# Kernel tuning notes

Hardware: AMD Instinct MI355X
Metric: run time of the kernel (lower is better)

Reference implementation:

```python
import jax, jax.numpy as jnp
import numpy as np

B, T, C, H = 2, 2048, 1024, 16
D = C // H

def setup_inputs() -> dict:
    key = jax.random.key(0)
    ks = jax.random.split(key, 8)
    s = 1.0 / np.sqrt(C)
    return {
        "x": jax.random.normal(ks[0], (B, T, C), dtype=jnp.float32),
        "Wk": jax.random.normal(ks[1], (C, C), dtype=jnp.float32) * s,
        "Wq": jax.random.normal(ks[2], (C, C), dtype=jnp.float32) * s,
        "bq": jax.random.normal(ks[3], (C,), dtype=jnp.float32) * 0.02,
        "Wv": jax.random.normal(ks[4], (C, C), dtype=jnp.float32) * s,
        "bv": jax.random.normal(ks[5], (C,), dtype=jnp.float32) * 0.02,
        "Wo": jax.random.normal(ks[6], (C, C), dtype=jnp.float32) * s,
        "bo": jax.random.normal(ks[7], (C,), dtype=jnp.float32) * 0.02,
    }

def reference(x, Wk, Wq, bq, Wv, bv, Wo, bo):
    b, t, c = x.shape
    # projections (key has no bias, matching nn.Linear(bias=False))
    q = (x @ Wq.T + bq).reshape(b, t, H, D).transpose(0, 2, 1, 3)  # [B,H,T,D]
    k = (x @ Wk.T).reshape(b, t, H, D).transpose(0, 2, 1, 3)
    v = (x @ Wv.T + bv).reshape(b, t, H, D).transpose(0, 2, 1, 3)
    scale = D ** -0.5
    attn = jnp.einsum('bhqd,bhkd->bhqk', q, k) * scale  # [B,H,T,T]
    causal = jnp.tril(jnp.ones((t, t), dtype=bool))
    attn = jnp.where(causal[None, None], attn, -jnp.inf)
    attn = jax.nn.softmax(attn, axis=-1)
    y = jnp.einsum('bhqk,bhkd->bhqd', attn, v)  # [B,H,T,D]
    y = y.transpose(0, 2, 1, 3).reshape(b, t, c)
    return y @ Wo.T + bo
```

## Files before the change

### kernel.cpp

```cpp
#include <hip/hip_runtime.h>
#include <hip/hip_bf16.h>
#include <stdint.h>

#define B_ 2
#define T_ 2048
#define C_ 1024
#define H_ 16
#define D_ 64
#define M_ (B_ * T_)

typedef __bf16 bf16x8 __attribute__((ext_vector_type(8)));
typedef float f32x4 __attribute__((ext_vector_type(4)));
typedef float f32x16 __attribute__((ext_vector_type(16)));

__device__ inline void gload_lds16(const void* g, void* l) {
  __builtin_amdgcn_global_load_lds(
      (const __attribute__((address_space(1))) void*)g,
      (__attribute__((address_space(3))) void*)l, 16, 0, 0);
}

__global__ __launch_bounds__(256) void cvt_all(
    const float* __restrict__ x, const float* __restrict__ Wq,
    const float* __restrict__ Wk, const float* __restrict__ Wv,
    const float* __restrict__ Wo, __hip_bfloat16* __restrict__ xb,
    __hip_bfloat16* __restrict__ wqb, __hip_bfloat16* __restrict__ wkb,
    __hip_bfloat16* __restrict__ wvb, __hip_bfloat16* __restrict__ wob) {
  size_t t = (size_t)blockIdx.x * 256 + threadIdx.x;
  size_t e = t * 4;
  const float* src;
  __hip_bfloat16* dst;
  size_t off;
  if (e < 4194304) {
    src = x; dst = xb; off = e;
  } else {
    size_t u = e - 4194304;
    int seg = (int)(u >> 20);
    off = u & 1048575;
    src = (seg == 0) ? Wq : (seg == 1) ? Wk : (seg == 2) ? Wv : Wo;
    dst = (seg == 0) ? wqb : (seg == 1) ? wkb : (seg == 2) ? wvb : wob;
  }
  float4 v = *(const float4*)(src + off);
  union { __hip_bfloat16 h[4]; ushort4 u4; } cv;
  cv.h[0] = __float2bfloat16(v.x);
  cv.h[1] = __float2bfloat16(v.y);
  cv.h[2] = __float2bfloat16(v.z);
  cv.h[3] = __float2bfloat16(v.w);
  *(ushort4*)(dst + off) = cv.u4;
}

__global__ __launch_bounds__(256) void gemm_qkv(
    const __hip_bfloat16* __restrict__ X,
    const __hip_bfloat16* __restrict__ Wq,
    const __hip_bfloat16* __restrict__ Wk,
    const __hip_bfloat16* __restrict__ Wv,
    const float* __restrict__ bq, const float* __restrict__ bv,
    __hip_bfloat16* __restrict__ Qo, __hip_bfloat16* __restrict__ Ko,
    __hip_bfloat16* __restrict__ VTo) {
  const int z = blockIdx.z;
  const int bx = ((blockIdx.x & 3) << 3) | (blockIdx.x >> 2);
  const __hip_bfloat16* Amat;
  const __hip_bfloat16* Bmat;
  int bm, bn;
  if (z == 2) {
    Amat = Wv; Bmat = X; bm = blockIdx.y; bn = bx;
  } else {
    Amat = X; Bmat = (z == 0) ? Wq : Wk; bm = bx; bn = blockIdx.y;
  }

  const int tid = threadIdx.x;
  const int w = tid >> 6, lane = tid & 63;
  const int wr = w >> 1, wc = w & 1;
  const int lrow = lane & 15, lk = (lane >> 4) * 8;

  __shared__ __hip_bfloat16 As[128 * 32];
  __shared__ __hip_bfloat16 Bs[128 * 32];

  f32x4 acc[4][4];
#pragma unroll
  for (int m = 0; m < 4; ++m)
#pragma unroll
    for (int n = 0; n < 4; ++n) acc[m][n] = (f32x4){0.f, 0.f, 0.f, 0.f};

  for (int k0 = 0; k0 < C_; k0 += 32) {
#pragma unroll
    for (int it = 0; it < 2; ++it) {
      int e = it * 2048 + w * 512 + lane * 8;
      int row = e >> 5, col = e & 31;
      gload_lds16(Amat + (size_t)(bm * 128 + row) * C_ + k0 + col, &As[e]);
      gload_lds16(Bmat + (size_t)(bn * 128 + row) * C_ + k0 + col, &Bs[e]);
    }
    asm volatile("s_waitcnt vmcnt(0)" ::: "memory");
    __syncthreads();

    bf16x8 af[4], bfr[4];
#pragma unroll
    for (int m = 0; m < 4; ++m)
      af[m] = *(const bf16x8*)&As[(wr * 64 + m * 16 + lrow) * 32 + lk];
#pragma unroll
    for (int n = 0; n < 4; ++n)
      bfr[n] = *(const bf16x8*)&Bs[(wc * 64 + n * 16 + lrow) * 32 + lk];
#pragma unroll
    for (int m = 0; m < 4; ++m)
#pragma unroll
      for (int n = 0; n < 4; ++n)
        acc[m][n] = __builtin_amdgcn_mfma_f32_16x16x32_bf16(af[m], bfr[n],
                                                            acc[m][n], 0, 0, 0);
    __syncthreads();
  }

#pragma unroll
  for (int m = 0; m < 4; ++m) {
#pragma unroll
    for (int n = 0; n < 4; ++n) {
      f32x4 v = acc[m][n];
      int rowm = bm * 128 + wr * 64 + m * 16 + (lane >> 4) * 4;
      int coln = bn * 128 + wc * 64 + n * 16 + (lane & 15);
      if (z == 2) {
        int b = coln >> 11, tl = coln & 2047;
#pragma unroll
        for (int r = 0; r < 4; ++r) {
          int rc = rowm + r;
          int h = rc >> 6, d = rc & 63;
          VTo[(((size_t)(b * H_ + h)) * D_ + d) * T_ + tl] =
              __float2bfloat16(v[r] + bv[rc]);
        }
      } else {
        float bb = (z == 0) ? bq[coln] : 0.f;
        float sc = (z == 0) ? 0.125f : 1.0f;
        int h = coln >> 6, d = coln & 63;
        __hip_bfloat16* Out = (z == 0) ? Qo : Ko;
#pragma unroll
        for (int r = 0; r < 4; ++r) {
          int row = rowm + r;
          int b = row >> 11, t = row & 2047;
          Out[(((size_t)(b * H_ + h)) * T_ + t) * D_ + d] =
              __float2bfloat16((v[r] + bb) * sc);
        }
      }
    }
  }
}

__global__ __launch_bounds__(256) void gemm_out(
    const __hip_bfloat16* __restrict__ X,
    const __hip_bfloat16* __restrict__ W,
    const float* __restrict__ bias, float* __restrict__ Out) {
  const int bm = ((blockIdx.x & 3) << 3) | (blockIdx.x >> 2);
  const int bn = blockIdx.y;
  const int tid = threadIdx.x;
  const int w = tid >> 6, lane = tid & 63;
  const int wr = w >> 1, wc = w & 1;
  const int lrow = lane & 15, lk = (lane >> 4) * 8;

  __shared__ __hip_bfloat16 As[128 * 32];
  __shared__ __hip_bfloat16 Bs[128 * 32];

  f32x4 acc[4][4];
#pragma unroll
  for (int m = 0; m < 4; ++m)
#pragma unroll
    for (int n = 0; n < 4; ++n) acc[m][n] = (f32x4){0.f, 0.f, 0.f, 0.f};

  for (int k0 = 0; k0 < C_; k0 += 32) {
#pragma unroll
    for (int it = 0; it < 2; ++it) {
      int e = it * 2048 + w * 512 + lane * 8;
      int row = e >> 5, col = e & 31;
      gload_lds16(X + (size_t)(bm * 128 + row) * C_ + k0 + col, &As[e]);
      gload_lds16(W + (size_t)(bn * 128 + row) * C_ + k0 + col, &Bs[e]);
    }
    asm volatile("s_waitcnt vmcnt(0)" ::: "memory");
    __syncthreads();

    bf16x8 af[4], bfr[4];
#pragma unroll
    for (int m = 0; m < 4; ++m)
      af[m] = *(const bf16x8*)&As[(wr * 64 + m * 16 + lrow) * 32 + lk];
#pragma unroll
    for (int n = 0; n < 4; ++n)
      bfr[n] = *(const bf16x8*)&Bs[(wc * 64 + n * 16 + lrow) * 32 + lk];
#pragma unroll
    for (int m = 0; m < 4; ++m)
#pragma unroll
      for (int n = 0; n < 4; ++n)
        acc[m][n] = __builtin_amdgcn_mfma_f32_16x16x32_bf16(af[m], bfr[n],
                                                            acc[m][n], 0, 0, 0);
    __syncthreads();
  }

#pragma unroll
  for (int m = 0; m < 4; ++m) {
#pragma unroll
    for (int n = 0; n < 4; ++n) {
      f32x4 v = acc[m][n];
      int coln = bn * 128 + wc * 64 + n * 16 + (lane & 15);
      float bb = bias[coln];
#pragma unroll
      for (int r = 0; r < 4; ++r) {
        int row = bm * 128 + wr * 64 + m * 16 + (lane >> 4) * 4 + r;
        Out[(size_t)row * C_ + coln] = v[r] + bb;
      }
    }
  }
}

#define MASKV_ -1e30f
#define MFLOOR_ -30000.0f
#define THR_ 8.0f

__global__ __launch_bounds__(512, 4) void attn_fwd(
    const __hip_bfloat16* __restrict__ Q, const __hip_bfloat16* __restrict__ K,
    const __hip_bfloat16* __restrict__ VT, __hip_bfloat16* __restrict__ Y) {
  const int qt = (gridDim.x - 1) - blockIdx.x;
  const int bh = blockIdx.y;
  const int tid = threadIdx.x;
  const int wid = tid >> 6, lane = tid & 63;
  const int g = wid >> 2, wq = wid & 3;
  const int hi = lane >> 5, q32 = lane & 31;
  const size_t base = (size_t)bh * T_ * D_;

  __shared__ __align__(16) char smem[65536 + 2048];
  auto KsP = (__hip_bfloat16(*)[64][64])(smem);
  auto VtsP = (__hip_bfloat16(*)[64][64])(smem + 32768);
  float* Sml = (float*)(smem + 65536);
  float(*Om)[32][68] = (float(*)[32][68])(smem);

  const int qg = qt * 128 + wq * 32 + q32;

  bf16x8 qf[4];
#pragma unroll
  for (int dk = 0; dk < 4; ++dk)
    qf[dk] = *(const bf16x8*)&Q[base + (size_t)qg * D_ + dk * 16 + hi * 8];

  f32x16 o0 = {}, o1 = {};
  float m_run = MFLOOR_, l_run = 0.f;

  const int gt = tid & 255;
  const int srow = gt >> 3, scnk = gt & 7;
  const int swz = (scnk ^ (srow & 7)) * 8;

#define STAGE(buf, kt)                                                      \
  {                                                                         \
    _Pragma("unroll") for (int h2 = 0; h2 < 2; ++h2) {                      \
      int row = srow + 32 * h2;                                             \
      gload_lds16(K + base + (size_t)((kt)*64 + row) * D_ + swz,            \
                  &KsP[g * 2 + (buf)][row][scnk * 8]);                      \
      gload_lds16(VT + base + (size_t)row * T_ + (kt)*64 + swz,             \
                  &VtsP[g * 2 + (buf)][row][scnk * 8]);                     \
    }                                                                       \
  }

  STAGE(0, g);
  asm volatile("s_waitcnt vmcnt(0)" ::: "memory");
  __syncthreads();

  int cur = 0;
  for (int s = 0; s <= qt; ++s) {
    const int kt = 2 * s + g;
    if (s < qt) STAGE(cur ^ 1, 2 * (s + 1) + g);

    f32x16 st0 = {}, st1 = {};
    __builtin_amdgcn_s_setprio(1);
#pragma unroll
    for (int dk = 0; dk < 4; ++dk) {
      int off = (dk * 16 + hi * 8) ^ ((lane & 7) << 3);
      bf16x8 a0 = *(const bf16x8*)&KsP[g * 2 + cur][q32][off];
      bf16x8 a1 = *(const bf16x8*)&KsP[g * 2 + cur][q32 + 32][off];
      st0 = __builtin_amdgcn_mfma_f32_32x32x16_bf16(a0, qf[dk], st0, 0, 0, 0);
      st1 = __builtin_amdgcn_mfma_f32_32x32x16_bf16(a1, qf[dk], st1, 0, 0, 0);
    }
    __builtin_amdgcn_s_setprio(0);

    float sc[32];
#pragma unroll
    for (int r = 0; r < 16; ++r) {
      sc[r] = st0[r];
      sc[16 + r] = st1[r];
    }
    if (s == qt) {
#pragma unroll
      for (int r = 0; r < 16; ++r) {
        int kvl = (r & 3) + 8 * (r >> 2) + 4 * hi;
        if (kt * 64 + kvl > qg) sc[r] = MASKV_;
        if (kt * 64 + 32 + kvl > qg) sc[16 + r] = MASKV_;
      }
    }
    float mt = sc[0];
#pragma unroll
    for (int r = 1; r < 32; ++r) mt = fmaxf(mt, sc[r]);
    mt = fmaxf(mt, __shfl_xor(mt, 32));
    if (__any(mt - m_run > THR_)) {
      float m_new = fmaxf(m_run, mt);
      float alpha = __expf(m_run - m_new);
      m_run = m_new;
      l_run *= alpha;
#pragma unroll
      for (int r = 0; r < 16; ++r) {
        o0[r] *= alpha;
        o1[r] *= alpha;
      }
    }
    float ls = 0.f;
#pragma unroll
    for (int r = 0; r < 32; ++r) {
      float p = __expf(sc[r] - m_run);
      sc[r] = p;
      ls += p;
    }
    ls += __shfl_xor(ls, 32);
    l_run += ls;

    __builtin_amdgcn_s_setprio(1);
#pragma unroll
    for (int ks = 0; ks < 4; ++ks) {
      union { unsigned w[4]; bf16x8 v; } pa;
      unsigned A, Bb;
      asm("v_cvt_pk_bf16_f32 %0, %1, %2"
          : "=v"(A) : "v"(sc[ks * 8 + 0]), "v"(sc[ks * 8 + 1]));
      asm("v_cvt_pk_bf16_f32 %0, %1, %2"
          : "=v"(Bb) : "v"(sc[ks * 8 + 4]), "v"(sc[ks * 8 + 5]));
      asm volatile("v_permlane32_swap_b32 %0, %1" : "+v"(A), "+v"(Bb));
      pa.w[0] = A;
      pa.w[2] = Bb;
      asm("v_cvt_pk_bf16_f32 %0, %1, %2"
          : "=v"(A) : "v"(sc[ks * 8 + 2]), "v"(sc[ks * 8 + 3]));
      asm("v_cvt_pk_bf16_f32 %0, %1, %2"
          : "=v"(Bb) : "v"(sc[ks * 8 + 6]), "v"(sc[ks * 8 + 7]));
      asm volatile("v_permlane32_swap_b32 %0, %1" : "+v"(A), "+v"(Bb));
      pa.w[1] = A;
      pa.w[3] = Bb;

      int voff = (ks * 16 + hi * 8) ^ ((lane & 7) << 3);
      bf16x8 v0 = *(const bf16x8*)&VtsP[g * 2 + cur][q32][voff];
      bf16x8 v1 = *(const bf16x8*)&VtsP[g * 2 + cur][q32 + 32][voff];
      o0 = __builtin_amdgcn_mfma_f32_32x32x16_bf16(v0, pa.v, o0, 0, 0, 0);
      o1 = __builtin_amdgcn_mfma_f32_32x32x16_bf16(v1, pa.v, o1, 0, 0, 0);
    }
    __builtin_amdgcn_s_setprio(0);

    asm volatile("s_waitcnt vmcnt(0)" ::: "memory");
    __syncthreads();
    cur ^= 1;
  }

  if (lane < 32) {
    Sml[((g * 4 + wq) * 2 + 0) * 32 + lane] = m_run;
    Sml[((g * 4 + wq) * 2 + 1) * 32 + lane] = l_run;
  }
  __syncthreads();
  float mo = Sml[(((1 - g) * 4 + wq) * 2 + 0) * 32 + q32];
  float lo_ = Sml[(((1 - g) * 4 + wq) * 2 + 1) * 32 + q32];
  float mstar = fmaxf(m_run, mo);
  float f = __expf(m_run - mstar);
  float fo = __expf(mo - mstar);
  float lstar = l_run * f + lo_ * fo;

  if (g == 1) {
#pragma unroll
    for (int dt = 0; dt < 2; ++dt) {
#pragma unroll
      for (int grp = 0; grp < 4; ++grp) {
        int dbase = grp * 8 + hi * 4 + dt * 32;
        float4 t4;
        t4.x = (dt ? o1[grp * 4 + 0] : o0[grp * 4 + 0]) * f;
        t4.y = (dt ? o1[grp * 4 + 1] : o0[grp * 4 + 1]) * f;
        t4.z = (dt ? o1[grp * 4 + 2] : o0[grp * 4 + 2]) * f;
        t4.w = (dt ? o1[grp * 4 + 3] : o0[grp * 4 + 3]) * f;
        *(float4*)&Om[wq][q32][dbase] = t4;
      }
    }
  }
  __syncthreads();
  if (g == 0) {
    float inv = 1.0f / lstar;
    const int b = bh >> 4, hh = bh & 15;
#pragma unroll
    for (int dt = 0; dt < 2; ++dt) {
#pragma unroll
      for (int grp = 0; grp < 4; ++grp) {
        int dbase = grp * 8 + hi * 4 + dt * 32;
        float4 m4 = *(float4*)&Om[wq][q32][dbase];
        union { __hip_bfloat16 h4[4]; ushort4 u; } pk;
        float e0 = (dt ? o1[grp * 4 + 0] : o0[grp * 4 + 0]) * f + m4.x;
        float e1 = (dt ? o1[grp * 4 + 1] : o0[grp * 4 + 1]) * f + m4.y;
        float e2 = (dt ? o1[grp * 4 + 2] : o0[grp * 4 + 2]) * f + m4.z;
        float e3 = (dt ? o1[grp * 4 + 3] : o0[grp * 4 + 3]) * f + m4.w;
        pk.h4[0] = __float2bfloat16(e0 * inv);
        pk.h4[1] = __float2bfloat16(e1 * inv);
        pk.h4[2] = __float2bfloat16(e2 * inv);
        pk.h4[3] = __float2bfloat16(e3 * inv);
        *(ushort4*)&Y[((size_t)b * T_ + qg) * C_ + hh * 64 + dbase] = pk.u;
      }
    }
  }
}

extern "C" void kernel_launch(void* const* d_in, const int* in_sizes, int n_in,
                              void* d_out, int out_size, void* d_ws,
                              size_t ws_size, hipStream_t stream) {
  const float* x = (const float*)d_in[0];
  const float* Wk = (const float*)d_in[1];
  const float* Wq = (const float*)d_in[2];
  const float* bq = (const float*)d_in[3];
  const float* Wv = (const float*)d_in[4];
  const float* bv = (const float*)d_in[5];
  const float* Wo = (const float*)d_in[6];
  const float* bo = (const float*)d_in[7];
  float* out = (float*)d_out;

  char* ws = (char*)d_ws;
  __hip_bfloat16* xb = (__hip_bfloat16*)(ws);
  __hip_bfloat16* wqb = (__hip_bfloat16*)(ws + (8ull << 20));
  __hip_bfloat16* wkb = (__hip_bfloat16*)(ws + (10ull << 20));
  __hip_bfloat16* wvb = (__hip_bfloat16*)(ws + (12ull << 20));
  __hip_bfloat16* wob = (__hip_bfloat16*)(ws + (14ull << 20));
  __hip_bfloat16* Qb = (__hip_bfloat16*)(ws + (16ull << 20));
  __hip_bfloat16* Kb = (__hip_bfloat16*)(ws + (24ull << 20));
  __hip_bfloat16* VTb = (__hip_bfloat16*)(ws + (32ull << 20));
  __hip_bfloat16* Yb = (__hip_bfloat16*)(ws + (40ull << 20));

  cvt_all<<<8192, 256, 0, stream>>>(x, Wq, Wk, Wv, Wo, xb, wqb, wkb, wvb, wob);
  gemm_qkv<<<dim3(32, 8, 3), 256, 0, stream>>>(xb, wqb, wkb, wvb, bq, bv, Qb,
                                               Kb, VTb);
  attn_fwd<<<dim3(16, 32), 512, 0, stream>>>(Qb, Kb, VTb, Yb);
  gemm_out<<<dim3(32, 8), 256, 0, stream>>>(Yb, wob, bo, out);
}
```

Measured before the change: 118.6 us.

## Pair causal query tiles per block and switch softmax to exp2 domain

Each attention block now processes two query tiles, j and 15-j, so every block does an equal amount of causal work. The grid shrinks from 512 to 256 blocks and the launch bound drops to 2 blocks per SM. The Q scale now folds in log2(e), so the softmax uses exp2 directly and the rescale threshold is adjusted to match. Fewer blocks may leave the GPU less occupied, and shared memory is now declared as separate arrays rather than as a single aliased buffer.

```diff
diff --git a/kernel.cpp b/kernel.cpp
--- a/kernel.cpp
+++ b/kernel.cpp
@@ -126,7 +126,7 @@
         }
       } else {
         float bb = (z == 0) ? bq[coln] : 0.f;
-        float sc = (z == 0) ? 0.125f : 1.0f;
+        float sc = (z == 0) ? 0.18033688011112042f : 1.0f;
         int h = coln >> 6, d = coln & 63;
         __hip_bfloat16* Out = (z == 0) ? Qo : Ko;
 #pragma unroll
@@ -206,34 +206,24 @@
 
 #define MASKV_ -1e30f
 #define MFLOOR_ -30000.0f
-#define THR_ 8.0f
-
-__global__ __launch_bounds__(512, 4) void attn_fwd(
+#define THR2_ 11.54f
+
+__global__ __launch_bounds__(512, 2) void attn_fwd(
     const __hip_bfloat16* __restrict__ Q, const __hip_bfloat16* __restrict__ K,
     const __hip_bfloat16* __restrict__ VT, __hip_bfloat16* __restrict__ Y) {
-  const int qt = (gridDim.x - 1) - blockIdx.x;
-  const int bh = blockIdx.y;
+  const int bh = blockIdx.x;
+  const int j = blockIdx.y;
   const int tid = threadIdx.x;
   const int wid = tid >> 6, lane = tid & 63;
   const int g = wid >> 2, wq = wid & 3;
   const int hi = lane >> 5, q32 = lane & 31;
   const size_t base = (size_t)bh * T_ * D_;
-
-  __shared__ __align__(16) char smem[65536 + 2048];
-  auto KsP = (__hip_bfloat16(*)[64][64])(smem);
-  auto VtsP = (__hip_bfloat16(*)[64][64])(smem + 32768);
-  float* Sml = (float*)(smem + 65536);
-  float(*Om)[32][68] = (float(*)[32][68])(smem);
-
-  const int qg = qt * 128 + wq * 32 + q32;
-
-  bf16x8 qf[4];
-#pragma unroll
-  for (int dk = 0; dk < 4; ++dk)
-    qf[dk] = *(const bf16x8*)&Q[base + (size_t)qg * D_ + dk * 16 + hi * 8];
-
-  f32x16 o0 = {}, o1 = {};
-  float m_run = MFLOOR_, l_run = 0.f;
+  const int b = bh >> 4, hh = bh & 15;
+
+  __shared__ __hip_bfloat16 Ks[2][2][64][64];
+  __shared__ __hip_bfloat16 Vts[2][2][64][64];
+  __shared__ float Sml[2][4][2][32];
+  __shared__ float Om[4][32][68];
 
   const int gt = tid & 255;
   const int srow = gt >> 3, scnk = gt & 7;
@@ -244,154 +234,167 @@
     _Pragma("unroll") for (int h2 = 0; h2 < 2; ++h2) {                      \
       int row = srow + 32 * h2;                                             \
       gload_lds16(K + base + (size_t)((kt)*64 + row) * D_ + swz,            \
-                  &KsP[g * 2 + (buf)][row][scnk * 8]);                      \
+                  &Ks[g][(buf)][row][scnk * 8]);                            \
       gload_lds16(VT + base + (size_t)row * T_ + (kt)*64 + swz,             \
-                  &VtsP[g * 2 + (buf)][row][scnk * 8]);                     \
+                  &Vts[g][(buf)][row][scnk * 8]);                           \
     }                                                                       \
   }
 
-  STAGE(0, g);
-  asm volatile("s_waitcnt vmcnt(0)" ::: "memory");
-  __syncthreads();
-
-  int cur = 0;
-  for (int s = 0; s <= qt; ++s) {
-    const int kt = 2 * s + g;
-    if (s < qt) STAGE(cur ^ 1, 2 * (s + 1) + g);
-
-    f32x16 st0 = {}, st1 = {};
-    __builtin_amdgcn_s_setprio(1);
-#pragma unroll
-    for (int dk = 0; dk < 4; ++dk) {
-      int off = (dk * 16 + hi * 8) ^ ((lane & 7) << 3);
-      bf16x8 a0 = *(const bf16x8*)&KsP[g * 2 + cur][q32][off];
-      bf16x8 a1 = *(const bf16x8*)&KsP[g * 2 + cur][q32 + 32][off];
-      st0 = __builtin_amdgcn_mfma_f32_32x32x16_bf16(a0, qf[dk], st0, 0, 0, 0);
-      st1 = __builtin_amdgcn_mfma_f32_32x32x16_bf16(a1, qf[dk], st1, 0, 0, 0);
-    }
-    __builtin_amdgcn_s_setprio(0);
-
-    float sc[32];
-#pragma unroll
-    for (int r = 0; r < 16; ++r) {
-      sc[r] = st0[r];
-      sc[16 + r] = st1[r];
-    }
-    if (s == qt) {
+  for (int ph = 0; ph < 2; ++ph) {
+    const int qt = ph ? (15 - j) : j;
+    const int qg = qt * 128 + wq * 32 + q32;
+
+    bf16x8 qf[4];
+#pragma unroll
+    for (int dk = 0; dk < 4; ++dk)
+      qf[dk] = *(const bf16x8*)&Q[base + (size_t)qg * D_ + dk * 16 + hi * 8];
+
+    f32x16 o0 = {}, o1 = {};
+    float m_run = MFLOOR_, l_run = 0.f;
+
+    STAGE(0, g);
+    asm volatile("s_waitcnt vmcnt(0)" ::: "memory");
+    __syncthreads();
+
+    int cur = 0;
+    for (int s = 0; s <= qt; ++s) {
+      const int kt = 2 * s + g;
+      if (s < qt) STAGE(cur ^ 1, 2 * (s + 1) + g);
+
+      f32x16 st0 = {}, st1 = {};
+      __builtin_amdgcn_s_setprio(1);
+#pragma unroll
+      for (int dk = 0; dk < 4; ++dk) {
+        int off = (dk * 16 + hi * 8) ^ ((lane & 7) << 3);
+        bf16x8 a0 = *(const bf16x8*)&Ks[g][cur][q32][off];
+        bf16x8 a1 = *(const bf16x8*)&Ks[g][cur][q32 + 32][off];
+        st0 = __builtin_amdgcn_mfma_f32_32x32x16_bf16(a0, qf[dk], st0, 0, 0, 0);
+        st1 = __builtin_amdgcn_mfma_f32_32x32x16_bf16(a1, qf[dk], st1, 0, 0, 0);
+      }
+      __builtin_amdgcn_s_setprio(0);
+
+      float sc[32];
 #pragma unroll
       for (int r = 0; r < 16; ++r) {
-        int kvl = (r & 3) + 8 * (r >> 2) + 4 * hi;
-        if (kt * 64 + kvl > qg) sc[r] = MASKV_;
-        if (kt * 64 + 32 + kvl > qg) sc[16 + r] = MASKV_;
-      }
-    }
-    float mt = sc[0];
-#pragma unroll
-    for (int r = 1; r < 32; ++r) mt = fmaxf(mt, sc[r]);
-    mt = fmaxf(mt, __shfl_xor(mt, 32));
-    if (__any(mt - m_run > THR_)) {
-      float m_new = fmaxf(m_run, mt);
-      float alpha = __expf(m_run - m_new);
-      m_run = m_new;
-      l_run *= alpha;
-#pragma unroll
-      for (int r = 0; r < 16; ++r) {
-        o0[r] *= alpha;
-        o1[r] *= alpha;
-      }
-    }
-    float ls = 0.f;
-#pragma unroll
-    for (int r = 0; r < 32; ++r) {
-      float p = __expf(sc[r] - m_run);
-      sc[r] = p;
-      ls += p;
-    }
-    ls += __shfl_xor(ls, 32);
-    l_run += ls;
-
-    __builtin_amdgcn_s_setprio(1);
-#pragma unroll
-    for (int ks = 0; ks < 4; ++ks) {
-      union { unsigned w[4]; bf16x8 v; } pa;
-      unsigned A, Bb;
-      asm("v_cvt_pk_bf16_f32 %0, %1, %2"
-          : "=v"(A) : "v"(sc[ks * 8 + 0]), "v"(sc[ks * 8 + 1]));
-      asm("v_cvt_pk_bf16_f32 %0, %1, %2"
-          : "=v"(Bb) : "v"(sc[ks * 8 + 4]), "v"(sc[ks * 8 + 5]));
-      asm volatile("v_permlane32_swap_b32 %0, %1" : "+v"(A), "+v"(Bb));
-      pa.w[0] = A;
-      pa.w[2] = Bb;
-      asm("v_cvt_pk_bf16_f32 %0, %1, %2"
-          : "=v"(A) : "v"(sc[ks * 8 + 2]), "v"(sc[ks * 8 + 3]));
-      asm("v_cvt_pk_bf16_f32 %0, %1, %2"
-          : "=v"(Bb) : "v"(sc[ks * 8 + 6]), "v"(sc[ks * 8 + 7]));
-      asm volatile("v_permlane32_swap_b32 %0, %1" : "+v"(A), "+v"(Bb));
-      pa.w[1] = A;
-      pa.w[3] = Bb;
-
-      int voff = (ks * 16 + hi * 8) ^ ((lane & 7) << 3);
-      bf16x8 v0 = *(const bf16x8*)&VtsP[g * 2 + cur][q32][voff];
-      bf16x8 v1 = *(const bf16x8*)&VtsP[g * 2 + cur][q32 + 32][voff];
-      o0 = __builtin_amdgcn_mfma_f32_32x32x16_bf16(v0, pa.v, o0, 0, 0, 0);
-      o1 = __builtin_amdgcn_mfma_f32_32x32x16_bf16(v1, pa.v, o1, 0, 0, 0);
-    }
-    __builtin_amdgcn_s_setprio(0);
-
-    asm volatile("s_waitcnt vmcnt(0)" ::: "memory");
-    __syncthreads();
-    cur ^= 1;
-  }
-
-  if (lane < 32) {
-    Sml[((g * 4 + wq) * 2 + 0) * 32 + lane] = m_run;
-    Sml[((g * 4 + wq) * 2 + 1) * 32 + lane] = l_run;
-  }
-  __syncthreads();
-  float mo = Sml[(((1 - g) * 4 + wq) * 2 + 0) * 32 + q32];
-  float lo_ = Sml[(((1 - g) * 4 + wq) * 2 + 1) * 32 + q32];
-  float mstar = fmaxf(m_run, mo);
-  float f = __expf(m_run - mstar);
-  float fo = __expf(mo - mstar);
-  float lstar = l_run * f + lo_ * fo;
-
-  if (g == 1) {
-#pragma unroll
-    for (int dt = 0; dt < 2; ++dt) {
-#pragma unroll
-      for (int grp = 0; grp < 4; ++grp) {
-        int dbase = grp * 8 + hi * 4 + dt * 32;
-        float4 t4;
-        t4.x = (dt ? o1[grp * 4 + 0] : o0[grp * 4 + 0]) * f;
-        t4.y = (dt ? o1[grp * 4 + 1] : o0[grp * 4 + 1]) * f;
-        t4.z = (dt ? o1[grp * 4 + 2] : o0[grp * 4 + 2]) * f;
-        t4.w = (dt ? o1[grp * 4 + 3] : o0[grp * 4 + 3]) * f;
-        *(float4*)&Om[wq][q32][dbase] = t4;
-      }
-    }
-  }
-  __syncthreads();
-  if (g == 0) {
-    float inv = 1.0f / lstar;
-    const int b = bh >> 4, hh = bh & 15;
-#pragma unroll
-    for (int dt = 0; dt < 2; ++dt) {
-#pragma unroll
-      for (int grp = 0; grp < 4; ++grp) {
-        int dbase = grp * 8 + hi * 4 + dt * 32;
-        float4 m4 = *(float4*)&Om[wq][q32][dbase];
-        union { __hip_bfloat16 h4[4]; ushort4 u; } pk;
-        float e0 = (dt ? o1[grp * 4 + 0] : o0[grp * 4 + 0]) * f + m4.x;
-        float e1 = (dt ? o1[grp * 4 + 1] : o0[grp * 4 + 1]) * f + m4.y;
-        float e2 = (dt ? o1[grp * 4 + 2] : o0[grp * 4 + 2]) * f + m4.z;
-        float e3 = (dt ? o1[grp * 4 + 3] : o0[grp * 4 + 3]) * f + m4.w;
-        pk.h4[0] = __float2bfloat16(e0 * inv);
-        pk.h4[1] = __float2bfloat16(e1 * inv);
-        pk.h4[2] = __float2bfloat16(e2 * inv);
-        pk.h4[3] = __float2bfloat16(e3 * inv);
-        *(ushort4*)&Y[((size_t)b * T_ + qg) * C_ + hh * 64 + dbase] = pk.u;
-      }
-    }
+        sc[r] = st0[r];
+        sc[16 + r] = st1[r];
+      }
+      if (s == qt) {
+#pragma unroll
+        for (int r = 0; r < 16; ++r) {
+          int kvl = (r & 3) + 8 * (r >> 2) + 4 * hi;
+          if (kt * 64 + kvl > qg) sc[r] = MASKV_;
+          if (kt * 64 + 32 + kvl > qg) sc[16 + r] = MASKV_;
+        }
+      }
+      float mt = sc[0];
+#pragma unroll
+      for (int r = 1; r < 32; ++r) mt = fmaxf(mt, sc[r]);
+      mt = fmaxf(mt, __shfl_xor(mt, 32));
+      if (__any(mt - m_run > THR2_)) {
+        float m_new = fmaxf(m_run, mt);
+        float alpha = __builtin_exp2f(m_run - m_new);
+        m_run = m_new;
+        l_run *= alpha;
+#pragma unroll
+        for (int r = 0; r < 16; ++r) {
+          o0[r] *= alpha;
+          o1[r] *= alpha;
+        }
+      }
+      float ls = 0.f;
+#pragma unroll
+      for (int r = 0; r < 32; ++r) {
+        float p = __builtin_exp2f(sc[r] - m_run);
+        sc[r] = p;
+        ls += p;
+      }
+      ls += __shfl_xor(ls, 32);
+      l_run += ls;
+
+      __builtin_amdgcn_s_setprio(1);
+#pragma unroll
+      for (int ks = 0; ks < 4; ++ks) {
+        union { unsigned w[4]; bf16x8 v; } pa;
+        unsigned A, Bb;
+        asm("v_cvt_pk_bf16_f32 %0, %1, %2"
+            : "=v"(A) : "v"(sc[ks * 8 + 0]), "v"(sc[ks * 8 + 1]));
+        asm("v_cvt_pk_bf16_f32 %0, %1, %2"
+            : "=v"(Bb) : "v"(sc[ks * 8 + 4]), "v"(sc[ks * 8 + 5]));
+        asm volatile("v_permlane32_swap_b32 %0, %1" : "+v"(A), "+v"(Bb));
+        pa.w[0] = A;
+        pa.w[2] = Bb;
+        asm("v_cvt_pk_bf16_f32 %0, %1, %2"
+            : "=v"(A) : "v"(sc[ks * 8 + 2]), "v"(sc[ks * 8 + 3]));
+        asm("v_cvt_pk_bf16_f32 %0, %1, %2"
+            : "=v"(Bb) : "v"(sc[ks * 8 + 6]), "v"(sc[ks * 8 + 7]));
+        asm volatile("v_permlane32_swap_b32 %0, %1" : "+v"(A), "+v"(Bb));
+        pa.w[1] = A;
+        pa.w[3] = Bb;
+
+        int voff = (ks * 16 + hi * 8) ^ ((lane & 7) << 3);
+        bf16x8 v0 = *(const bf16x8*)&Vts[g][cur][q32][voff];
+        bf16x8 v1 = *(const bf16x8*)&Vts[g][cur][q32 + 32][voff];
+        o0 = __builtin_amdgcn_mfma_f32_32x32x16_bf16(v0, pa.v, o0, 0, 0, 0);
+        o1 = __builtin_amdgcn_mfma_f32_32x32x16_bf16(v1, pa.v, o1, 0, 0, 0);
+      }
+      __builtin_amdgcn_s_setprio(0);
+
+      asm volatile("s_waitcnt vmcnt(0)" ::: "memory");
+      __syncthreads();
+      cur ^= 1;
+    }
+
+    if (lane < 32) {
+      Sml[g][wq][0][lane] = m_run;
+      Sml[g][wq][1][lane] = l_run;
+    }
+    __syncthreads();
+    float mo = Sml[1 - g][wq][0][q32];
+    float lo_ = Sml[1 - g][wq][1][q32];
+    float mstar = fmaxf(m_run, mo);
+    float f = __builtin_exp2f(m_run - mstar);
+    float fo = __builtin_exp2f(mo - mstar);
+    float lstar = l_run * f + lo_ * fo;
+
+    if (g == 1) {
+#pragma unroll
+      for (int dt = 0; dt < 2; ++dt) {
+#pragma unroll
+        for (int grp = 0; grp < 4; ++grp) {
+          int dbase = grp * 8 + hi * 4 + dt * 32;
+          float4 t4;
+          t4.x = (dt ? o1[grp * 4 + 0] : o0[grp * 4 + 0]) * f;
+          t4.y = (dt ? o1[grp * 4 + 1] : o0[grp * 4 + 1]) * f;
+          t4.z = (dt ? o1[grp * 4 + 2] : o0[grp * 4 + 2]) * f;
+          t4.w = (dt ? o1[grp * 4 + 3] : o0[grp * 4 + 3]) * f;
+          *(float4*)&Om[wq][q32][dbase] = t4;
+        }
+      }
+    }
+    __syncthreads();
+    if (g == 0) {
+      float inv = 1.0f / lstar;
+#pragma unroll
+      for (int dt = 0; dt < 2; ++dt) {
+#pragma unroll
+        for (int grp = 0; grp < 4; ++grp) {
+          int dbase = grp * 8 + hi * 4 + dt * 32;
+          float4 m4 = *(float4*)&Om[wq][q32][dbase];
+          union { __hip_bfloat16 h4[4]; ushort4 u; } pk;
+          float e0 = (dt ? o1[grp * 4 + 0] : o0[grp * 4 + 0]) * f + m4.x;
+          float e1 = (dt ? o1[grp * 4 + 1] : o0[grp * 4 + 1]) * f + m4.y;
+          float e2 = (dt ? o1[grp * 4 + 2] : o0[grp * 4 + 2]) * f + m4.z;
+          float e3 = (dt ? o1[grp * 4 + 3] : o0[grp * 4 + 3]) * f + m4.w;
+          pk.h4[0] = __float2bfloat16(e0 * inv);
+          pk.h4[1] = __float2bfloat16(e1 * inv);
+          pk.h4[2] = __float2bfloat16(e2 * inv);
+          pk.h4[3] = __float2bfloat16(e3 * inv);
+          *(ushort4*)&Y[((size_t)b * T_ + qg) * C_ + hh * 64 + dbase] = pk.u;
+        }
+      }
+    }
+    __syncthreads();
   }
 }
 
@@ -422,6 +425,6 @@
   cvt_all<<<8192, 256, 0, stream>>>(x, Wq, Wk, Wv, Wo, xb, wqb, wkb, wvb, wob);
   gemm_qkv<<<dim3(32, 8, 3), 256, 0, stream>>>(xb, wqb, wkb, wvb, bq, bv, Qb,
                                                Kb, VTb);
-  attn_fwd<<<dim3(16, 32), 512, 0, stream>>>(Qb, Kb, VTb, Yb);
+  attn_fwd<<<dim3(32, 8), 512, 0, stream>>>(Qb, Kb, VTb, Yb);
   gemm_out<<<dim3(32, 8), 256, 0, stream>>>(Yb, wob, bo, out);
 }
```

Result: faster. 111.9 us (-5.7%).
